# Kernel optimization log

Hardware: AMD Instinct MI355X
Metric: run time of the kernel (lower is better)

## Reference

```python
import jax, jax.numpy as jnp
import numpy as np

NUM_USERS = 50000
NUM_ITEMS = 100000
NUM_NODES = NUM_USERS + NUM_ITEMS
LATENT_DIM = 64
N_LAYERS = 3
NNZ = 4800000
BATCH = 4096


def setup_inputs() -> dict:
    key = jax.random.key(0)
    ks = jax.random.split(key, 7)
    user_emb = 0.1 * jax.random.normal(ks[0], (NUM_USERS, LATENT_DIM), dtype=jnp.float32)
    item_emb = 0.1 * jax.random.normal(ks[1], (NUM_ITEMS, LATENT_DIM), dtype=jnp.float32)
    edge_rows = jnp.sort(jax.random.randint(ks[2], (NNZ,), 0, NUM_NODES, dtype=jnp.int32))
    edge_cols = jax.random.randint(ks[3], (NNZ,), 0, NUM_NODES, dtype=jnp.int32)
    # degree-normalized-style positive edge values
    edge_vals = jax.random.uniform(ks[4], (NNZ,), dtype=jnp.float32)
    users = jax.random.randint(ks[5], (BATCH,), 0, NUM_USERS, dtype=jnp.int32)
    items = jax.random.randint(ks[6], (BATCH,), 0, NUM_ITEMS, dtype=jnp.int32)
    return {"user_emb": user_emb, "item_emb": item_emb,
            "edge_rows": edge_rows, "edge_cols": edge_cols, "edge_vals": edge_vals,
            "users": users, "items": items}


def _spmm(edge_rows, edge_cols, edge_vals, x):
    # out[r] = sum_{e: rows[e]==r} vals[e] * x[cols[e]]
    msgs = edge_vals[:, None] * x[edge_cols]        # [nnz, d]
    return jax.ops.segment_sum(msgs, edge_rows, num_segments=NUM_NODES)


def _computer(user_emb, item_emb, edge_rows, edge_cols, edge_vals):
    all_emb = jnp.concatenate([user_emb, item_emb], axis=0)  # [N, d]
    acc = all_emb
    cur = all_emb
    for _ in range(N_LAYERS):
        cur = _spmm(edge_rows, edge_cols, edge_vals, cur)
        acc = acc + cur
    light_out = acc / jnp.asarray(N_LAYERS + 1, dtype=all_emb.dtype)
    return light_out[:NUM_USERS], light_out[NUM_USERS:]


def reference(user_emb, item_emb, edge_rows, edge_cols, edge_vals, users, items):
    all_users, all_items = _computer(user_emb, item_emb, edge_rows, edge_cols, edge_vals)
    users_emb = all_users[users]   # [B, d]
    items_emb = all_items[items]   # [B, d]
    gamma = jnp.sum(users_emb * items_emb, axis=1)  # [B]
    return gamma
```

## Files before the change

### kernel.cpp

```cpp
#include <hip/hip_runtime.h>

#define NUM_USERS 50000
#define NUM_ITEMS 100000
#define NUM_NODES 150000
#define D 64
#define NNZ 4800000
#define BATCH 4096

typedef __attribute__((ext_vector_type(4))) _Float16 half4;

__global__ void k_init(const float* __restrict__ ue, const float* __restrict__ ie,
                       half4* __restrict__ cur, float* __restrict__ acc) {
    const int total = NUM_NODES * D / 4;
    const int ulim  = NUM_USERS * D / 4;
    const float4* u4 = (const float4*)ue;
    const float4* i4 = (const float4*)ie;
    float4* a4 = (float4*)acc;
    for (int i = blockIdx.x * blockDim.x + threadIdx.x; i < total;
         i += gridDim.x * blockDim.x) {
        float4 v = (i < ulim) ? u4[i] : i4[i - ulim];
        half4 h;
        h.x = (_Float16)v.x; h.y = (_Float16)v.y;
        h.z = (_Float16)v.z; h.w = (_Float16)v.w;
        cur[i] = h;
        a4[i] = v;
    }
}

__global__ void k_rowptr(const int* __restrict__ rows, int* __restrict__ rowptr) {
    int r = blockIdx.x * blockDim.x + threadIdx.x;
    if (r > NUM_NODES) return;
    int lo = 0, hi = NNZ;
    while (lo < hi) {
        int mid = (lo + hi) >> 1;
        if (rows[mid] < r) lo = mid + 1; else hi = mid;
    }
    rowptr[r] = lo;
}

template <bool WRITE_NEXT>
__global__ __launch_bounds__(256, 4) void k_spmm(const int* __restrict__ rowptr,
                       const int* __restrict__ cols,
                       const float* __restrict__ vals,
                       const half4* __restrict__ x,
                       half4* __restrict__ nxt,
                       float* __restrict__ acc) {
    const int wid   = (blockIdx.x * blockDim.x + threadIdx.x) >> 6;
    const int lane  = threadIdx.x & 63;
    const int l16   = lane & 15;
    const int gbase = lane & 48;
    const int row   = wid * 4 + (lane >> 4);
    if (row >= NUM_NODES) return;
    const int e0 = rowptr[row];
    const int e1 = rowptr[row + 1];
    float4 sum = make_float4(0.f, 0.f, 0.f, 0.f);

    int   idx0 = e0 + l16;
    bool  ok0  = idx0 < e1;
    int   myc  = ok0 ? cols[idx0] : 0;
    float myv  = ok0 ? vals[idx0] : 0.f;

    for (int e = e0; e < e1; e += 16) {
        int   c[16];
        float v[16];
#pragma unroll
        for (int t = 0; t < 16; ++t) {
            c[t] = __shfl(myc, gbase + t);
            v[t] = __shfl(myv, gbase + t);
        }
        {
            int  idx2 = e + 16 + l16;
            bool ok2  = idx2 < e1;
            myc = ok2 ? cols[idx2] : 0;
            myv = ok2 ? vals[idx2] : 0.f;
        }
        half4 xv[16];
#pragma unroll
        for (int t = 0; t < 16; ++t)
            xv[t] = x[(size_t)c[t] * 16 + l16];
        __builtin_amdgcn_sched_barrier(0);
#pragma unroll
        for (int t = 0; t < 16; ++t) {
            sum.x += v[t] * (float)xv[t].x;
            sum.y += v[t] * (float)xv[t].y;
            sum.z += v[t] * (float)xv[t].z;
            sum.w += v[t] * (float)xv[t].w;
        }
    }
    const size_t o = (size_t)row * 16 + l16;
    if (WRITE_NEXT) {
        half4 h;
        h.x = (_Float16)sum.x; h.y = (_Float16)sum.y;
        h.z = (_Float16)sum.z; h.w = (_Float16)sum.w;
        nxt[o] = h;
    }
    float4* acc4 = (float4*)acc;
    float4 a = acc4[o];
    a.x += sum.x; a.y += sum.y; a.z += sum.z; a.w += sum.w;
    acc4[o] = a;
}

__global__ void k_gamma(const float* __restrict__ acc,
                        const int* __restrict__ users,
                        const int* __restrict__ items,
                        float* __restrict__ out) {
    int wid  = (blockIdx.x * blockDim.x + threadIdx.x) >> 6;
    int lane = threadIdx.x & 63;
    if (wid >= BATCH) return;
    int u  = users[wid];
    int it = items[wid];
    float a = acc[(size_t)u * D + lane];
    float b = acc[((size_t)NUM_USERS + it) * D + lane];
    float p = a * b;
    for (int off = 32; off; off >>= 1) p += __shfl_down(p, off);
    if (lane == 0) out[wid] = p * (1.0f / 16.0f);
}

extern "C" void kernel_launch(void* const* d_in, const int* in_sizes, int n_in,
                              void* d_out, int out_size, void* d_ws, size_t ws_size,
                              hipStream_t stream) {
    const float* ue    = (const float*)d_in[0];
    const float* ie    = (const float*)d_in[1];
    const int*   rows  = (const int*)d_in[2];
    const int*   cols  = (const int*)d_in[3];
    const float* vals  = (const float*)d_in[4];
    const int*   users = (const int*)d_in[5];
    const int*   items = (const int*)d_in[6];
    float*       out   = (float*)d_out;

    char* ws = (char*)d_ws;
    size_t off = (((size_t)(NUM_NODES + 1) * sizeof(int)) + 255) & ~(size_t)255;
    const size_t halfbuf = (size_t)NUM_NODES * D * sizeof(_Float16);
    int*   rowptr = (int*)ws;
    half4* bufA   = (half4*)(ws + off);
    half4* bufB   = (half4*)(ws + off + halfbuf);
    float* acc    = (float*)(ws + off + 2 * halfbuf);

    k_rowptr<<<(NUM_NODES + 1 + 255) / 256, 256, 0, stream>>>(rows, rowptr);
    k_init<<<2048, 256, 0, stream>>>(ue, ie, bufA, acc);

    const int spmm_blocks = NUM_NODES / 16;
    k_spmm<true ><<<spmm_blocks, 256, 0, stream>>>(rowptr, cols, vals, bufA, bufB, acc);
    k_spmm<true ><<<spmm_blocks, 256, 0, stream>>>(rowptr, cols, vals, bufB, bufA, acc);
    k_spmm<false><<<spmm_blocks, 256, 0, stream>>>(rowptr, cols, vals, bufA, nullptr, acc);

    k_gamma<<<(BATCH * 64) / 256, 256, 0, stream>>>(acc, users, items, out);
}
```

Baseline: 295.9 us.

## Keep per-layer fp16 embeddings and sum layers only for batch rows in gamma

Drops the full-size fp32 accumulator that every SpMM layer read-modify-wrote; each layer now writes its fp16 output to its own buffer. The gamma kernel gathers the four layer embeddings for just the batched users and items and sums them there. This removes large per-layer accumulator traffic. In exchange, the layer-0 and final-layer contributions are held in fp16 rather than fp32, which slightly reduces precision.

Measured after the change: 263.4 us (median of 2 runs). -11.0%, faster.

```diff
diff --git a/kernel.cpp b/kernel.cpp
--- a/kernel.cpp
+++ b/kernel.cpp
@@ -10,20 +10,18 @@
 typedef __attribute__((ext_vector_type(4))) _Float16 half4;
 
 __global__ void k_init(const float* __restrict__ ue, const float* __restrict__ ie,
-                       half4* __restrict__ cur, float* __restrict__ acc) {
+                       half4* __restrict__ x0) {
     const int total = NUM_NODES * D / 4;
     const int ulim  = NUM_USERS * D / 4;
     const float4* u4 = (const float4*)ue;
     const float4* i4 = (const float4*)ie;
-    float4* a4 = (float4*)acc;
     for (int i = blockIdx.x * blockDim.x + threadIdx.x; i < total;
          i += gridDim.x * blockDim.x) {
         float4 v = (i < ulim) ? u4[i] : i4[i - ulim];
         half4 h;
         h.x = (_Float16)v.x; h.y = (_Float16)v.y;
         h.z = (_Float16)v.z; h.w = (_Float16)v.w;
-        cur[i] = h;
-        a4[i] = v;
+        x0[i] = h;
     }
 }
 
@@ -38,13 +36,11 @@
     rowptr[r] = lo;
 }
 
-template <bool WRITE_NEXT>
 __global__ __launch_bounds__(256, 4) void k_spmm(const int* __restrict__ rowptr,
                        const int* __restrict__ cols,
                        const float* __restrict__ vals,
                        const half4* __restrict__ x,
-                       half4* __restrict__ nxt,
-                       float* __restrict__ acc) {
+                       half4* __restrict__ nxt) {
     const int wid   = (blockIdx.x * blockDim.x + threadIdx.x) >> 6;
     const int lane  = threadIdx.x & 63;
     const int l16   = lane & 15;
@@ -87,33 +83,37 @@
             sum.w += v[t] * (float)xv[t].w;
         }
     }
-    const size_t o = (size_t)row * 16 + l16;
-    if (WRITE_NEXT) {
-        half4 h;
-        h.x = (_Float16)sum.x; h.y = (_Float16)sum.y;
-        h.z = (_Float16)sum.z; h.w = (_Float16)sum.w;
-        nxt[o] = h;
-    }
-    float4* acc4 = (float4*)acc;
-    float4 a = acc4[o];
-    a.x += sum.x; a.y += sum.y; a.z += sum.z; a.w += sum.w;
-    acc4[o] = a;
+    half4 h;
+    h.x = (_Float16)sum.x; h.y = (_Float16)sum.y;
+    h.z = (_Float16)sum.z; h.w = (_Float16)sum.w;
+    nxt[(size_t)row * 16 + l16] = h;
 }
 
-__global__ void k_gamma(const float* __restrict__ acc,
-                        const int* __restrict__ users,
-                        const int* __restrict__ items,
+__global__ void k_gamma(const half4* __restrict__ x0, const half4* __restrict__ x1,
+                        const half4* __restrict__ x2, const half4* __restrict__ x3,
+                        const int* __restrict__ users, const int* __restrict__ items,
                         float* __restrict__ out) {
-    int wid  = (blockIdx.x * blockDim.x + threadIdx.x) >> 6;
-    int lane = threadIdx.x & 63;
-    if (wid >= BATCH) return;
-    int u  = users[wid];
-    int it = items[wid];
-    float a = acc[(size_t)u * D + lane];
-    float b = acc[((size_t)NUM_USERS + it) * D + lane];
-    float p = a * b;
-    for (int off = 32; off; off >>= 1) p += __shfl_down(p, off);
-    if (lane == 0) out[wid] = p * (1.0f / 16.0f);
+    const int wid  = (blockIdx.x * blockDim.x + threadIdx.x) >> 6;
+    const int lane = threadIdx.x & 63;
+    const int l16  = lane & 15;
+    const int b    = wid * 4 + (lane >> 4);
+    if (b >= BATCH) return;
+    const size_t ur = (size_t)users[b] * 16 + l16;
+    const size_t ir = ((size_t)NUM_USERS + items[b]) * 16 + l16;
+    half4 a0 = x0[ur], a1 = x1[ur], a2 = x2[ur], a3 = x3[ur];
+    half4 c0 = x0[ir], c1 = x1[ir], c2 = x2[ir], c3 = x3[ir];
+    float p = 0.f;
+#pragma unroll
+    for (int j = 0; j < 4; ++j) {
+        float su = (float)a0[j] + (float)a1[j] + (float)a2[j] + (float)a3[j];
+        float si = (float)c0[j] + (float)c1[j] + (float)c2[j] + (float)c3[j];
+        p += su * si;
+    }
+    p += __shfl_xor(p, 8);
+    p += __shfl_xor(p, 4);
+    p += __shfl_xor(p, 2);
+    p += __shfl_xor(p, 1);
+    if (l16 == 0) out[b] = p * (1.0f / 16.0f);
 }
 
 extern "C" void kernel_launch(void* const* d_in, const int* in_sizes, int n_in,
@@ -132,17 +132,18 @@
     size_t off = (((size_t)(NUM_NODES + 1) * sizeof(int)) + 255) & ~(size_t)255;
     const size_t halfbuf = (size_t)NUM_NODES * D * sizeof(_Float16);
     int*   rowptr = (int*)ws;
-    half4* bufA   = (half4*)(ws + off);
-    half4* bufB   = (half4*)(ws + off + halfbuf);
-    float* acc    = (float*)(ws + off + 2 * halfbuf);
+    half4* x0     = (half4*)(ws + off);
+    half4* x1     = (half4*)(ws + off + 1 * halfbuf);
+    half4* x2     = (half4*)(ws + off + 2 * halfbuf);
+    half4* x3     = (half4*)(ws + off + 3 * halfbuf);
 
     k_rowptr<<<(NUM_NODES + 1 + 255) / 256, 256, 0, stream>>>(rows, rowptr);
-    k_init<<<2048, 256, 0, stream>>>(ue, ie, bufA, acc);
+    k_init<<<2048, 256, 0, stream>>>(ue, ie, x0);
 
     const int spmm_blocks = NUM_NODES / 16;
-    k_spmm<true ><<<spmm_blocks, 256, 0, stream>>>(rowptr, cols, vals, bufA, bufB, acc);
-    k_spmm<true ><<<spmm_blocks, 256, 0, stream>>>(rowptr, cols, vals, bufB, bufA, acc);
-    k_spmm<false><<<spmm_blocks, 256, 0, stream>>>(rowptr, cols, vals, bufA, nullptr, acc);
+    k_spmm<<<spmm_blocks, 256, 0, stream>>>(rowptr, cols, vals, x0, x1);
+    k_spmm<<<spmm_blocks, 256, 0, stream>>>(rowptr, cols, vals, x1, x2);
+    k_spmm<<<spmm_blocks, 256, 0, stream>>>(rowptr, cols, vals, x2, x3);
 
-    k_gamma<<<(BATCH * 64) / 256, 256, 0, stream>>>(acc, users, items, out);
+    k_gamma<<<BATCH / 16, 256, 0, stream>>>(x0, x1, x2, x3, users, items, out);
 }
```
